# Optimization experiments

Hardware: AMD Instinct MI355X
Metric: run time of the kernel (lower is better)

The kernel has to match this reference:

```python
import jax, jax.numpy as jnp
import numpy as np

# dims: R ranks, B batch, HQ q-heads, HKV kv-heads-per-rank, G = HQ//HKV group size,
# D head dim, S kv splits (hardcoded 32 in module), L max kv len per rank, P pages per rank
R, B, HQ, HKV, D, S, L, P = 4, 16, 32, 2, 128, 32, 2048, 32768
G = HQ // HKV  # kv_group_num = num_q_heads // num_kv_heads_per_rank
NEG = -jnp.inf


def setup_inputs() -> dict:
    key = jax.random.key(0)
    k1, k2, k3, k4, k5 = jax.random.split(key, 5)
    q = jax.random.normal(k1, (B, HQ, D), jnp.float32)
    k_cache = jax.random.normal(k2, (R, P, HKV, D), jnp.float32)
    v_cache = jax.random.normal(k3, (R, P, HKV, D), jnp.float32)
    block_table = jax.random.randint(k4, (R, B, L), 0, P, jnp.int32)
    # per-rank kv lengths; min 64 to keep all math well-defined
    kv_lens_per_rank = jax.random.randint(k5, (R, B), 64, L + 1, jnp.int32)
    return dict(q=q, k_cache=k_cache, v_cache=v_cache,
                block_table=block_table, kv_lens_per_rank=kv_lens_per_rank)


def _attend(q, k_cache, v_cache, block_table, kv_lens):
    scale = D ** -0.5
    # page_size == 1: block_table entries are token slots in the per-rank cache.
    ridx = jnp.arange(R)[:, None, None]
    k = k_cache[ridx, block_table]  # [R,B,L,HKV,D]
    v = v_cache[ridx, block_table]  # [R,B,L,HKV,D]

    # GQA: q head h uses local kv head h // G on each rank
    qg = q.reshape(B, HKV, G, D)
    scores = jnp.einsum('bkgd,rblkd->rbkgl', qg, k) * scale  # [R,B,HKV,G,L]

    n = jnp.arange(L)
    valid = n[None, None, :] < kv_lens[..., None]            # [R,B,L]
    scores = jnp.where(valid[:, :, None, None, :], scores, NEG)

    # stage 1: split-KV. split s covers [s*per, (s+1)*per) with per = ceil(len/S)
    per = -(-kv_lens // S)                                   # [R,B]
    sid = n[None, None, :] // per[..., None]                 # [R,B,L]

    lse_s = []
    for s in range(S):  # fixed small loop over NUM_KV_SPLITS
        m = jnp.where((sid == s)[:, :, None, None, :], scores, NEG)
        lse_s.append(jax.scipy.special.logsumexp(m, axis=-1))  # [R,B,HKV,G]
    lse_s = jnp.stack(lse_s)  # [S,R,B,HKV,G]; empty splits -> -inf (kernel skips them)

    # stage 2: local combine over splits. NOTE (faithful to kernel): local_out stores
    # the UNNORMALIZED accumulator sum_s exp(lse_s - m_r) * o_s together with
    # lse_r = m_r + log(sum_s exp(lse_s - m_r)), where m_r = max_s lse_s.
    m_r = jnp.max(lse_s, axis=0)                              # [R,B,HKV,G]
    lse_r = m_r + jnp.log(jnp.sum(jnp.exp(lse_s - m_r), axis=0))
    # sum_s exp(lse_s - m_r) * (softmax_s @ v_s) == sum_n exp(score_n - m_r) * v_n
    p = jnp.exp(scores - m_r[..., None])                      # masked entries -> 0
    acc_r = jnp.einsum('rbkgl,rblkd->rbkgd', p, v)            # [R,B,HKV,G,D]

    acc = acc_r.reshape(R, B, HQ, D)
    lse = lse_r.reshape(R, B, HQ)

    # stage 3: global lse-weighted combine across ranks (online softmax == this)
    M = jnp.max(lse, axis=0)                                  # [B,HQ]
    w = jnp.exp(lse - M)                                      # [R,B,HQ]
    out = jnp.sum(w[..., None] * acc, axis=0) / jnp.sum(w, axis=0)[..., None]
    return out  # [B,HQ,D]


def reference(q, k_cache, v_cache, block_table, kv_lens_per_rank):
    return _attend(q, k_cache, v_cache, block_table, kv_lens_per_rank)
```

## Files before the change

### kernel.cpp

```cpp
#include <hip/hip_runtime.h>
#include <math.h>

#define R_ 4
#define B_ 16
#define HQ_ 32
#define HKV_ 2
#define G_ 16
#define D_ 128
#define S_ 32
#define L_ 2048
#define P_ 32768
#define TS_ 64
#define KSTR 136
#define PSTR 18
#define NEGINF (-INFINITY)

typedef _Float16 h4 __attribute__((ext_vector_type(4)));
typedef _Float16 h8 __attribute__((ext_vector_type(8)));
typedef float    fx4 __attribute__((ext_vector_type(4)));


__global__ __launch_bounds__(256, 8) void fd_stage1(
    const float* __restrict__ q, const float* __restrict__ kc,
    const float* __restrict__ vc, const int* __restrict__ bt,
    const int* __restrict__ lens,
    float* __restrict__ lse_split, float* __restrict__ chunk_m,
    _Float16* __restrict__ chunk_acc)
{
  const int t   = threadIdx.x;
  const int blk = blockIdx.x;
  const int s   = blk & 31;
  const int hkv = (blk >> 5) & 1;
  const int b   = (blk >> 6) & 15;
  const int r   = blk >> 10;

  const int len = lens[r*B_ + b];
  const int per = (len + 31) >> 5;
  const int n0  = s*per;
  const int tn  = min(per, len - n0);

  float* lse_out = lse_split + ((r*B_ + b)*HKV_ + hkv)*(S_*G_);
  const int cmbase = (((r*B_ + b)*HKV_ + hkv)*S_ + s)*G_;
  _Float16* ca = chunk_acc + (size_t)(((r*B_ + b)*HKV_ + hkv)*S_ + s)*(G_*D_);

  if (tn <= 0) {
    if (t < G_) { lse_out[s*G_ + t] = NEGINF; chunk_m[cmbase + t] = NEGINF; }
    h8 z = {};
    *(h8*)&ca[t*8] = z;
    return;
  }

  __shared__ _Float16 q_s[G_][KSTR];
  __shared__ __align__(16) float p_s[TS_][PSTR];
  __shared__ int pg_s[TS_];
  __shared__ float2 red_s[64];

  const int* btb   = bt + (r*B_ + b)*L_;
  const int kvbase = r*(P_*HKV_*D_) + hkv*D_;

  if (t < TS_) pg_s[t] = btb[n0 + t];

  {
    const float* qb = q + (b*HQ_ + hkv*G_)*D_;
    int fi = t;
    #pragma unroll
    for (int i = 0; i < 2; ++i, fi += 256) {
      const int g = fi >> 5, dd = (fi & 31)*4;
      const float4 v = *(const float4*)&qb[g*D_ + dd];
      h4 hv; hv.x=(_Float16)v.x; hv.y=(_Float16)v.y; hv.z=(_Float16)v.z; hv.w=(_Float16)v.w;
      *(h4*)&q_s[g][dd] = hv;
    }
  }
  __syncthreads();

  const int w  = t >> 6;
  const int l  = t & 63;
  const int hh = l & 15;
  const int tq = l >> 4;
  const bool active = (16*w) < tn;

  fx4 dacc = {0.f, 0.f, 0.f, 0.f};
  if (active) {
    const int row = 16*w + hh;
    const int pg  = pg_s[row];
    const float* kr = kc + kvbase + pg*(HKV_*D_) + 8*tq;
    #pragma unroll
    for (int c = 0; c < 4; ++c) {
      const float4 f0 = *(const float4*)&kr[c*32];
      const float4 f1 = *(const float4*)&kr[c*32 + 4];
      h8 af;
      af[0]=(_Float16)f0.x; af[1]=(_Float16)f0.y; af[2]=(_Float16)f0.z; af[3]=(_Float16)f0.w;
      af[4]=(_Float16)f1.x; af[5]=(_Float16)f1.y; af[6]=(_Float16)f1.z; af[7]=(_Float16)f1.w;
      const h8 bf = *(const h8*)&q_s[hh][c*32 + 8*tq];
      dacc = __builtin_amdgcn_mfma_f32_16x16x32_f16(af, bf, dacc, 0, 0, 0);
    }
  }

  const float sc = 0.08838834764831845f;
  const int nb = 16*w + 4*tq;
  const float sv0 = (nb + 0 < tn) ? dacc[0]*sc : NEGINF;
  const float sv1 = (nb + 1 < tn) ? dacc[1]*sc : NEGINF;
  const float sv2 = (nb + 2 < tn) ? dacc[2]*sc : NEGINF;
  const float sv3 = (nb + 3 < tn) ? dacc[3]*sc : NEGINF;

  float pmw = fmaxf(fmaxf(sv0, sv1), fmaxf(sv2, sv3));
  pmw = fmaxf(pmw, __shfl_xor(pmw, 16));
  pmw = fmaxf(pmw, __shfl_xor(pmw, 32));
  const float pms = (pmw == NEGINF) ? 0.f : pmw;
  const float e0 = __expf(sv0 - pms);
  const float e1 = __expf(sv1 - pms);
  const float e2 = __expf(sv2 - pms);
  const float e3 = __expf(sv3 - pms);
  float psw = e0 + e1 + e2 + e3;
  psw += __shfl_xor(psw, 16);
  psw += __shfl_xor(psw, 32);

  if (l < 16) red_s[w*16 + l] = make_float2(pmw, psw);
  __syncthreads();

  const float2 rr0 = red_s[hh], rr1 = red_s[16 + hh];
  const float2 rr2 = red_s[32 + hh], rr3 = red_s[48 + hh];
  const float pm = fmaxf(fmaxf(rr0.x, rr1.x), fmaxf(rr2.x, rr3.x));
  const float ps = rr0.y*__expf(rr0.x - pm) + rr1.y*__expf(rr1.x - pm)
                 + rr2.y*__expf(rr2.x - pm) + rr3.y*__expf(rr3.x - pm);

  if (w == 0 && l < 16) {
    lse_out[s*G_ + l]   = pm + __logf(ps);
    chunk_m[cmbase + l] = pm;
  }

  if (active) {
    const float cw = __expf(pmw - pm);
    p_s[nb + 0][hh] = e0*cw;
    p_s[nb + 1][hh] = e1*cw;
    p_s[nb + 2][hh] = e2*cw;
    p_s[nb + 3][hh] = e3*cw;
  }
  __syncthreads();

  const int d4 = (t & 31)*4;
  const int g2 = (t >> 5)*2;
  float4 a0 = make_float4(0.f,0.f,0.f,0.f);
  float4 a1 = make_float4(0.f,0.f,0.f,0.f);
  #pragma unroll 4
  for (int n = 0; n < tn; ++n) {
    const int pg = pg_s[n];
    const float4 v4 = *(const float4*)&vc[kvbase + pg*(HKV_*D_) + d4];
    const float2 pp = *(const float2*)&p_s[n][g2];
    a0.x += pp.x*v4.x; a0.y += pp.x*v4.y; a0.z += pp.x*v4.z; a0.w += pp.x*v4.w;
    a1.x += pp.y*v4.x; a1.y += pp.y*v4.y; a1.z += pp.y*v4.z; a1.w += pp.y*v4.w;
  }

  h4 o0; o0.x=(_Float16)a0.x; o0.y=(_Float16)a0.y; o0.z=(_Float16)a0.z; o0.w=(_Float16)a0.w;
  h4 o1; o1.x=(_Float16)a1.x; o1.y=(_Float16)a1.y; o1.z=(_Float16)a1.z; o1.w=(_Float16)a1.w;
  *(h4*)&ca[g2*D_ + d4]       = o0;
  *(h4*)&ca[(g2 + 1)*D_ + d4] = o1;
}

__global__ __launch_bounds__(128) void fd_stage2(
    const float* __restrict__ lse_split, const float* __restrict__ chunk_m,
    const _Float16* __restrict__ chunk_acc, float* __restrict__ out)
{
  const int bh  = blockIdx.x;
  const int b   = bh >> 5, h = bh & 31;
  const int hkv = h >> 4, g = h & 15;
  const int d   = threadIdx.x;

  float m_r[R_], lse_r[R_];
  #pragma unroll
  for (int r = 0; r < R_; ++r) {
    const float* ls = lse_split + ((r*B_ + b)*HKV_ + hkv)*(S_*G_) + g;
    float m = NEGINF;
    #pragma unroll 8
    for (int s2 = 0; s2 < S_; ++s2) m = fmaxf(m, ls[s2*G_]);
    float sum = 0.f;
    #pragma unroll 8
    for (int s2 = 0; s2 < S_; ++s2) sum += __expf(ls[s2*G_] - m);
    m_r[r]   = m;
    lse_r[r] = m + __logf(sum);
  }
  const float M = fmaxf(fmaxf(lse_r[0], lse_r[1]), fmaxf(lse_r[2], lse_r[3]));
  float denom = 0.f, o = 0.f;
  #pragma unroll
  for (int r = 0; r < R_; ++r) {
    const float w = __expf(lse_r[r] - M);
    denom += w;
    const float* cm = chunk_m + (((r*B_ + b)*HKV_ + hkv)*S_)*G_ + g;
    const _Float16* ca = chunk_acc
        + (size_t)(((r*B_ + b)*HKV_ + hkv)*S_)*(G_*D_) + g*D_ + d;
    float a = 0.f;
    #pragma unroll 8
    for (int c = 0; c < S_; ++c)
      a += __expf(cm[c*G_] - m_r[r]) * (float)ca[(size_t)c*(G_*D_)];
    o += w * a;
  }
  out[(size_t)bh*D_ + d] = o / denom;
}

extern "C" void kernel_launch(void* const* d_in, const int* in_sizes, int n_in,
                              void* d_out, int out_size, void* d_ws, size_t ws_size,
                              hipStream_t stream) {
  const float* q   = (const float*)d_in[0];
  const float* kc  = (const float*)d_in[1];
  const float* vc  = (const float*)d_in[2];
  const int*   bt  = (const int*)d_in[3];
  const int*   len = (const int*)d_in[4];
  float* out = (float*)d_out;
  float* ws  = (float*)d_ws;

  const size_t lse_f = (size_t)R_*B_*HKV_*S_*G_;
  float*    lse_split = ws;
  float*    chunk_m   = ws + lse_f;
  _Float16* chunk_acc = (_Float16*)(ws + 2*lse_f);

  fd_stage1<<<dim3(R_*B_*HKV_*S_), dim3(256), 0, stream>>>(
      q, kc, vc, bt, len, lse_split, chunk_m, chunk_acc);
  fd_stage2<<<dim3(B_*HQ_), dim3(128), 0, stream>>>(
      lse_split, chunk_m, chunk_acc, out);
}
```

Measured before the change: 300.5 us.

## Process both KV heads per stage-1 block to share page gathers

Stage 1 now handles both local KV heads in one block instead of one block per head, halving the grid. Each gathered page row is read for both heads at once, so K and V loads become contiguous 2×128 float spans and the block-table and page-index loads are shared. The cost is twice the MFMA and softmax work and more shared memory and registers per block, which may reduce occupancy and parallelism. A row bounds guard is added to the K loads.

```diff
diff --git a/kernel.cpp b/kernel.cpp
--- a/kernel.cpp
+++ b/kernel.cpp
@@ -30,45 +30,54 @@
   const int t   = threadIdx.x;
   const int blk = blockIdx.x;
   const int s   = blk & 31;
-  const int hkv = (blk >> 5) & 1;
-  const int b   = (blk >> 6) & 15;
-  const int r   = blk >> 10;
+  const int b   = (blk >> 5) & 15;
+  const int r   = blk >> 9;
 
   const int len = lens[r*B_ + b];
   const int per = (len + 31) >> 5;
   const int n0  = s*per;
   const int tn  = min(per, len - n0);
 
-  float* lse_out = lse_split + ((r*B_ + b)*HKV_ + hkv)*(S_*G_);
-  const int cmbase = (((r*B_ + b)*HKV_ + hkv)*S_ + s)*G_;
-  _Float16* ca = chunk_acc + (size_t)(((r*B_ + b)*HKV_ + hkv)*S_ + s)*(G_*D_);
+  const int rb = r*B_ + b;
+  float* lse0 = lse_split + (rb*HKV_ + 0)*(S_*G_) + s*G_;
+  float* lse1 = lse_split + (rb*HKV_ + 1)*(S_*G_) + s*G_;
+  float* cm0  = chunk_m   + ((rb*HKV_ + 0)*S_ + s)*G_;
+  float* cm1  = chunk_m   + ((rb*HKV_ + 1)*S_ + s)*G_;
+  _Float16* ca0 = chunk_acc + (size_t)((rb*HKV_ + 0)*S_ + s)*(G_*D_);
+  _Float16* ca1 = chunk_acc + (size_t)((rb*HKV_ + 1)*S_ + s)*(G_*D_);
 
   if (tn <= 0) {
-    if (t < G_) { lse_out[s*G_ + t] = NEGINF; chunk_m[cmbase + t] = NEGINF; }
+    if (t < 32) {
+      const int hk = t >> 4, g = t & 15;
+      (hk ? lse1 : lse0)[g] = NEGINF;
+      (hk ? cm1  : cm0 )[g] = NEGINF;
+    }
     h8 z = {};
-    *(h8*)&ca[t*8] = z;
+    *(h8*)&ca0[t*8] = z;
+    *(h8*)&ca1[t*8] = z;
     return;
   }
 
-  __shared__ _Float16 q_s[G_][KSTR];
-  __shared__ __align__(16) float p_s[TS_][PSTR];
-  __shared__ int pg_s[TS_];
-  __shared__ float2 red_s[64];
-
-  const int* btb   = bt + (r*B_ + b)*L_;
-  const int kvbase = r*(P_*HKV_*D_) + hkv*D_;
+  __shared__ _Float16 q_s[2][G_][KSTR];
+  __shared__ float    p_s[2][TS_][PSTR];
+  __shared__ int      pg_s[TS_];
+  __shared__ float2   red_s[2][64];
+
+  const int* btb = bt + rb*L_;
+  const float* kcb = kc + (size_t)r*(P_*HKV_*D_);
+  const float* vcb = vc + (size_t)r*(P_*HKV_*D_);
 
   if (t < TS_) pg_s[t] = btb[n0 + t];
 
   {
-    const float* qb = q + (b*HQ_ + hkv*G_)*D_;
+    const float* qb = q + b*HQ_*D_;
     int fi = t;
     #pragma unroll
-    for (int i = 0; i < 2; ++i, fi += 256) {
-      const int g = fi >> 5, dd = (fi & 31)*4;
-      const float4 v = *(const float4*)&qb[g*D_ + dd];
+    for (int i = 0; i < 4; ++i, fi += 256) {
+      const int h32 = fi >> 5, dd = (fi & 31)*4;
+      const float4 v = *(const float4*)&qb[h32*D_ + dd];
       h4 hv; hv.x=(_Float16)v.x; hv.y=(_Float16)v.y; hv.z=(_Float16)v.z; hv.w=(_Float16)v.w;
-      *(h4*)&q_s[g][dd] = hv;
+      *(h4*)&q_s[h32 >> 4][h32 & 15][dd] = hv;
     }
   }
   __syncthreads();
@@ -79,82 +88,129 @@
   const int tq = l >> 4;
   const bool active = (16*w) < tn;
 
-  fx4 dacc = {0.f, 0.f, 0.f, 0.f};
+  fx4 d0 = {0.f,0.f,0.f,0.f}, d1 = {0.f,0.f,0.f,0.f};
   if (active) {
     const int row = 16*w + hh;
-    const int pg  = pg_s[row];
-    const float* kr = kc + kvbase + pg*(HKV_*D_) + 8*tq;
+    const bool rowok = row < tn;
+    const int pg = pg_s[row];
+    const float* kr = kcb + pg*(HKV_*D_) + 8*tq;
     #pragma unroll
     for (int c = 0; c < 4; ++c) {
-      const float4 f0 = *(const float4*)&kr[c*32];
-      const float4 f1 = *(const float4*)&kr[c*32 + 4];
-      h8 af;
-      af[0]=(_Float16)f0.x; af[1]=(_Float16)f0.y; af[2]=(_Float16)f0.z; af[3]=(_Float16)f0.w;
-      af[4]=(_Float16)f1.x; af[5]=(_Float16)f1.y; af[6]=(_Float16)f1.z; af[7]=(_Float16)f1.w;
-      const h8 bf = *(const h8*)&q_s[hh][c*32 + 8*tq];
-      dacc = __builtin_amdgcn_mfma_f32_16x16x32_f16(af, bf, dacc, 0, 0, 0);
+      h8 a0 = {}, a1 = {};
+      if (rowok) {
+        const float4 f0 = *(const float4*)&kr[c*32];
+        const float4 f1 = *(const float4*)&kr[c*32 + 4];
+        const float4 f2 = *(const float4*)&kr[D_ + c*32];
+        const float4 f3 = *(const float4*)&kr[D_ + c*32 + 4];
+        a0[0]=(_Float16)f0.x; a0[1]=(_Float16)f0.y; a0[2]=(_Float16)f0.z; a0[3]=(_Float16)f0.w;
+        a0[4]=(_Float16)f1.x; a0[5]=(_Float16)f1.y; a0[6]=(_Float16)f1.z; a0[7]=(_Float16)f1.w;
+        a1[0]=(_Float16)f2.x; a1[1]=(_Float16)f2.y; a1[2]=(_Float16)f2.z; a1[3]=(_Float16)f2.w;
+        a1[4]=(_Float16)f3.x; a1[5]=(_Float16)f3.y; a1[6]=(_Float16)f3.z; a1[7]=(_Float16)f3.w;
+      }
+      const h8 b0 = *(const h8*)&q_s[0][hh][c*32 + 8*tq];
+      const h8 b1 = *(const h8*)&q_s[1][hh][c*32 + 8*tq];
+      d0 = __builtin_amdgcn_mfma_f32_16x16x32_f16(a0, b0, d0, 0, 0, 0);
+      d1 = __builtin_amdgcn_mfma_f32_16x16x32_f16(a1, b1, d1, 0, 0, 0);
     }
   }
 
   const float sc = 0.08838834764831845f;
   const int nb = 16*w + 4*tq;
-  const float sv0 = (nb + 0 < tn) ? dacc[0]*sc : NEGINF;
-  const float sv1 = (nb + 1 < tn) ? dacc[1]*sc : NEGINF;
-  const float sv2 = (nb + 2 < tn) ? dacc[2]*sc : NEGINF;
-  const float sv3 = (nb + 3 < tn) ? dacc[3]*sc : NEGINF;
-
-  float pmw = fmaxf(fmaxf(sv0, sv1), fmaxf(sv2, sv3));
-  pmw = fmaxf(pmw, __shfl_xor(pmw, 16));
-  pmw = fmaxf(pmw, __shfl_xor(pmw, 32));
-  const float pms = (pmw == NEGINF) ? 0.f : pmw;
-  const float e0 = __expf(sv0 - pms);
-  const float e1 = __expf(sv1 - pms);
-  const float e2 = __expf(sv2 - pms);
-  const float e3 = __expf(sv3 - pms);
-  float psw = e0 + e1 + e2 + e3;
-  psw += __shfl_xor(psw, 16);
-  psw += __shfl_xor(psw, 32);
-
-  if (l < 16) red_s[w*16 + l] = make_float2(pmw, psw);
+  float pm0w, ps0w, pm1w, ps1w;
+  float e00,e01,e02,e03, e10,e11,e12,e13;
+  {
+    const float s00 = (nb+0 < tn) ? d0[0]*sc : NEGINF;
+    const float s01 = (nb+1 < tn) ? d0[1]*sc : NEGINF;
+    const float s02 = (nb+2 < tn) ? d0[2]*sc : NEGINF;
+    const float s03 = (nb+3 < tn) ? d0[3]*sc : NEGINF;
+    float pm = fmaxf(fmaxf(s00,s01), fmaxf(s02,s03));
+    pm = fmaxf(pm, __shfl_xor(pm, 16));
+    pm = fmaxf(pm, __shfl_xor(pm, 32));
+    const float pms = (pm == NEGINF) ? 0.f : pm;
+    e00 = __expf(s00 - pms); e01 = __expf(s01 - pms);
+    e02 = __expf(s02 - pms); e03 = __expf(s03 - pms);
+    float ps = e00 + e01 + e02 + e03;
+    ps += __shfl_xor(ps, 16); ps += __shfl_xor(ps, 32);
+    pm0w = pm; ps0w = ps;
+  }
+  {
+    const float s10 = (nb+0 < tn) ? d1[0]*sc : NEGINF;
+    const float s11 = (nb+1 < tn) ? d1[1]*sc : NEGINF;
+    const float s12 = (nb+2 < tn) ? d1[2]*sc : NEGINF;
+    const float s13 = (nb+3 < tn) ? d1[3]*sc : NEGINF;
+    float pm = fmaxf(fmaxf(s10,s11), fmaxf(s12,s13));
+    pm = fmaxf(pm, __shfl_xor(pm, 16));
+    pm = fmaxf(pm, __shfl_xor(pm, 32));
+    const float pms = (pm == NEGINF) ? 0.f : pm;
+    e10 = __expf(s10 - pms); e11 = __expf(s11 - pms);
+    e12 = __expf(s12 - pms); e13 = __expf(s13 - pms);
+    float ps = e10 + e11 + e12 + e13;
+    ps += __shfl_xor(ps, 16); ps += __shfl_xor(ps, 32);
+    pm1w = pm; ps1w = ps;
+  }
+
+  if (l < 16) {
+    red_s[0][w*16 + l] = make_float2(pm0w, ps0w);
+    red_s[1][w*16 + l] = make_float2(pm1w, ps1w);
+  }
   __syncthreads();
 
-  const float2 rr0 = red_s[hh], rr1 = red_s[16 + hh];
-  const float2 rr2 = red_s[32 + hh], rr3 = red_s[48 + hh];
-  const float pm = fmaxf(fmaxf(rr0.x, rr1.x), fmaxf(rr2.x, rr3.x));
-  const float ps = rr0.y*__expf(rr0.x - pm) + rr1.y*__expf(rr1.x - pm)
-                 + rr2.y*__expf(rr2.x - pm) + rr3.y*__expf(rr3.x - pm);
-
-  if (w == 0 && l < 16) {
-    lse_out[s*G_ + l]   = pm + __logf(ps);
-    chunk_m[cmbase + l] = pm;
+  float pm0, pm1;
+  {
+    const float2 a = red_s[0][hh], c2 = red_s[0][16+hh];
+    const float2 e2 = red_s[0][32+hh], g2r = red_s[0][48+hh];
+    pm0 = fmaxf(fmaxf(a.x,c2.x), fmaxf(e2.x,g2r.x));
+    const float ps = a.y*__expf(a.x-pm0) + c2.y*__expf(c2.x-pm0)
+                   + e2.y*__expf(e2.x-pm0) + g2r.y*__expf(g2r.x-pm0);
+    if (w == 0 && l < 16) { lse0[l] = pm0 + __logf(ps); cm0[l] = pm0; }
+  }
+  {
+    const float2 a = red_s[1][hh], c2 = red_s[1][16+hh];
+    const float2 e2 = red_s[1][32+hh], g2r = red_s[1][48+hh];
+    pm1 = fmaxf(fmaxf(a.x,c2.x), fmaxf(e2.x,g2r.x));
+    const float ps = a.y*__expf(a.x-pm1) + c2.y*__expf(c2.x-pm1)
+                   + e2.y*__expf(e2.x-pm1) + g2r.y*__expf(g2r.x-pm1);
+    if (w == 1 && l < 16) { lse1[l] = pm1 + __logf(ps); cm1[l] = pm1; }
   }
 
   if (active) {
-    const float cw = __expf(pmw - pm);
-    p_s[nb + 0][hh] = e0*cw;
-    p_s[nb + 1][hh] = e1*cw;
-    p_s[nb + 2][hh] = e2*cw;
-    p_s[nb + 3][hh] = e3*cw;
+    const float c0 = __expf(pm0w - pm0);
+    const float c1 = __expf(pm1w - pm1);
+    p_s[0][nb+0][hh] = e00*c0; p_s[0][nb+1][hh] = e01*c0;
+    p_s[0][nb+2][hh] = e02*c0; p_s[0][nb+3][hh] = e03*c0;
+    p_s[1][nb+0][hh] = e10*c1; p_s[1][nb+1][hh] = e11*c1;
+    p_s[1][nb+2][hh] = e12*c1; p_s[1][nb+3][hh] = e13*c1;
   }
   __syncthreads();
 
+  const int hk = (t >> 5) & 1;
   const int d4 = (t & 31)*4;
-  const int g2 = (t >> 5)*2;
-  float4 a0 = make_float4(0.f,0.f,0.f,0.f);
-  float4 a1 = make_float4(0.f,0.f,0.f,0.f);
-  #pragma unroll 4
+  const float* vb = vcb + hk*D_ + d4;
+  const float* pp = &p_s[hk][0][4*w];
+  float4 a0 = make_float4(0,0,0,0), a1 = make_float4(0,0,0,0);
+  float4 a2 = make_float4(0,0,0,0), a3 = make_float4(0,0,0,0);
+  #pragma unroll 2
   for (int n = 0; n < tn; ++n) {
     const int pg = pg_s[n];
-    const float4 v4 = *(const float4*)&vc[kvbase + pg*(HKV_*D_) + d4];
-    const float2 pp = *(const float2*)&p_s[n][g2];
-    a0.x += pp.x*v4.x; a0.y += pp.x*v4.y; a0.z += pp.x*v4.z; a0.w += pp.x*v4.w;
-    a1.x += pp.y*v4.x; a1.y += pp.y*v4.y; a1.z += pp.y*v4.z; a1.w += pp.y*v4.w;
-  }
-
-  h4 o0; o0.x=(_Float16)a0.x; o0.y=(_Float16)a0.y; o0.z=(_Float16)a0.z; o0.w=(_Float16)a0.w;
-  h4 o1; o1.x=(_Float16)a1.x; o1.y=(_Float16)a1.y; o1.z=(_Float16)a1.z; o1.w=(_Float16)a1.w;
-  *(h4*)&ca[g2*D_ + d4]       = o0;
-  *(h4*)&ca[(g2 + 1)*D_ + d4] = o1;
+    const float4 v4 = *(const float4*)&vb[pg*(HKV_*D_)];
+    const float2 p01 = *(const float2*)&pp[n*PSTR];
+    const float2 p23 = *(const float2*)&pp[n*PSTR + 2];
+    a0.x += p01.x*v4.x; a0.y += p01.x*v4.y; a0.z += p01.x*v4.z; a0.w += p01.x*v4.w;
+    a1.x += p01.y*v4.x; a1.y += p01.y*v4.y; a1.z += p01.y*v4.z; a1.w += p01.y*v4.w;
+    a2.x += p23.x*v4.x; a2.y += p23.x*v4.y; a2.z += p23.x*v4.z; a2.w += p23.x*v4.w;
+    a3.x += p23.y*v4.x; a3.y += p23.y*v4.y; a3.z += p23.y*v4.z; a3.w += p23.y*v4.w;
+  }
+
+  _Float16* ca = hk ? ca1 : ca0;
+  h4 o;
+  o.x=(_Float16)a0.x; o.y=(_Float16)a0.y; o.z=(_Float16)a0.z; o.w=(_Float16)a0.w;
+  *(h4*)&ca[(4*w+0)*D_ + d4] = o;
+  o.x=(_Float16)a1.x; o.y=(_Float16)a1.y; o.z=(_Float16)a1.z; o.w=(_Float16)a1.w;
+  *(h4*)&ca[(4*w+1)*D_ + d4] = o;
+  o.x=(_Float16)a2.x; o.y=(_Float16)a2.y; o.z=(_Float16)a2.z; o.w=(_Float16)a2.w;
+  *(h4*)&ca[(4*w+2)*D_ + d4] = o;
+  o.x=(_Float16)a3.x; o.y=(_Float16)a3.y; o.z=(_Float16)a3.z; o.w=(_Float16)a3.w;
+  *(h4*)&ca[(4*w+3)*D_ + d4] = o;
 }
 
 __global__ __launch_bounds__(128) void fd_stage2(
@@ -213,7 +269,7 @@
   float*    chunk_m   = ws + lse_f;
   _Float16* chunk_acc = (_Float16*)(ws + 2*lse_f);
 
-  fd_stage1<<<dim3(R_*B_*HKV_*S_), dim3(256), 0, stream>>>(
+  fd_stage1<<<dim3(R_*B_*S_), dim3(256), 0, stream>>>(
       q, kc, vc, bt, len, lse_split, chunk_m, chunk_acc);
   fd_stage2<<<dim3(B_*HQ_), dim3(128), 0, stream>>>(
       lse_split, chunk_m, chunk_acc, out);
```

After: 300.6 us. About the same (+0.0%).

## Split each KV split into two 32-token chunks with 128-thread blocks

Applied to the files above, without the earlier changes.

Stage 1 now launches twice as many blocks: each KV split is divided into two 32-token chunks handled by 128-thread blocks. Each block writes its raw max and exp-sum, and stage 2 combines the sub-chunks and recomputes the per-split LSE. This spreads the gather-bound work over more, smaller blocks and adds more index math and a larger workspace in stage 2. The new block-index order puts hkv and the rank/batch index in the low bits, and empty chunks now skip zeroing their accumulator, with stage 2 checking for -inf instead.

```diff
diff --git a/kernel.cpp b/kernel.cpp
--- a/kernel.cpp
+++ b/kernel.cpp
@@ -8,11 +8,11 @@
 #define G_ 16
 #define D_ 128
 #define S_ 32
+#define CT_ 32
 #define L_ 2048
 #define P_ 32768
-#define TS_ 64
 #define KSTR 136
-#define PSTR 18
+#define PSTR 20
 #define NEGINF (-INFINITY)
 
 typedef _Float16 h4 __attribute__((ext_vector_type(4)));
@@ -20,51 +20,54 @@
 typedef float    fx4 __attribute__((ext_vector_type(4)));
 
 
-__global__ __launch_bounds__(256, 8) void fd_stage1(
+__global__ __launch_bounds__(128, 6) void fd_stage1(
     const float* __restrict__ q, const float* __restrict__ kc,
     const float* __restrict__ vc, const int* __restrict__ bt,
     const int* __restrict__ lens,
-    float* __restrict__ lse_split, float* __restrict__ chunk_m,
+    float* __restrict__ pm_ws, float* __restrict__ se_ws,
     _Float16* __restrict__ chunk_acc)
 {
   const int t   = threadIdx.x;
   const int blk = blockIdx.x;
-  const int s   = blk & 31;
-  const int hkv = (blk >> 5) & 1;
-  const int b   = (blk >> 6) & 15;
-  const int r   = blk >> 10;
-
-  const int len = lens[r*B_ + b];
+  const int c   = blk >> 12;
+  const int s   = (blk >> 7) & 31;
+  const int rb  = (blk >> 1) & 63;
+  const int hkv = blk & 1;
+  const int r   = rb >> 4, b = rb & 15;
+
+  const int len = lens[rb];
   const int per = (len + 31) >> 5;
-  const int n0  = s*per;
-  const int tn  = min(per, len - n0);
-
-  float* lse_out = lse_split + ((r*B_ + b)*HKV_ + hkv)*(S_*G_);
-  const int cmbase = (((r*B_ + b)*HKV_ + hkv)*S_ + s)*G_;
-  _Float16* ca = chunk_acc + (size_t)(((r*B_ + b)*HKV_ + hkv)*S_ + s)*(G_*D_);
+  const int sn0 = s*per;
+  const int stn = min(per, len - sn0);
+  const int n0  = sn0 + c*CT_;
+  const int tn  = min(stn - c*CT_, CT_);
+
+  const int widx = ((rb*HKV_ + hkv)*S_ + s)*2 + c;
+  float* pm_out = pm_ws + widx*G_;
+  float* se_out = se_ws + widx*G_;
+  _Float16* ca  = chunk_acc + (size_t)widx*(G_*D_);
 
   if (tn <= 0) {
-    if (t < G_) { lse_out[s*G_ + t] = NEGINF; chunk_m[cmbase + t] = NEGINF; }
-    h8 z = {};
-    *(h8*)&ca[t*8] = z;
+    if (t < G_) { pm_out[t] = NEGINF; se_out[t] = 0.f; }
     return;
   }
 
   __shared__ _Float16 q_s[G_][KSTR];
-  __shared__ __align__(16) float p_s[TS_][PSTR];
-  __shared__ int pg_s[TS_];
-  __shared__ float2 red_s[64];
-
-  const int* btb   = bt + (r*B_ + b)*L_;
-  const int kvbase = r*(P_*HKV_*D_) + hkv*D_;
-
-  if (t < TS_) pg_s[t] = btb[n0 + t];
+  __shared__ __align__(16) float p_s[CT_][PSTR];
+  __shared__ int      pg_s[CT_];
+  __shared__ float2   red_s[2][G_];
+
+  const int* btb = bt + rb*L_;
+  const float* kvk = kc + (size_t)r*(P_*HKV_*D_) + hkv*D_;
+  const float* kvv = vc + (size_t)r*(P_*HKV_*D_) + hkv*D_;
+
+  if (t < CT_) pg_s[t] = btb[n0 + t];
 
   {
     const float* qb = q + (b*HQ_ + hkv*G_)*D_;
     int fi = t;
     #pragma unroll
-    for (int i = 0; i < 2; ++i, fi += 256) {
+    for (int i = 0; i < 4; ++i, fi += 128) {
       const int g = fi >> 5, dd = (fi & 31)*4;
       const float4 v = *(const float4*)&qb[g*D_ + dd];
       h4 hv; hv.x=(_Float16)v.x; hv.y=(_Float16)v.y; hv.z=(_Float16)v.z; hv.w=(_Float16)v.w;
@@ -79,29 +82,32 @@
   const int tq = l >> 4;
   const bool active = (16*w) < tn;
 
-  fx4 dacc = {0.f, 0.f, 0.f, 0.f};
+  fx4 d0 = {0.f,0.f,0.f,0.f};
   if (active) {
     const int row = 16*w + hh;
-    const int pg  = pg_s[row];
-    const float* kr = kc + kvbase + pg*(HKV_*D_) + 8*tq;
+    const bool rowok = row < tn;
+    const int pg = pg_s[row];
+    const float* kr = kvk + pg*(HKV_*D_) + 8*tq;
     #pragma unroll
-    for (int c = 0; c < 4; ++c) {
-      const float4 f0 = *(const float4*)&kr[c*32];
-      const float4 f1 = *(const float4*)&kr[c*32 + 4];
-      h8 af;
-      af[0]=(_Float16)f0.x; af[1]=(_Float16)f0.y; af[2]=(_Float16)f0.z; af[3]=(_Float16)f0.w;
-      af[4]=(_Float16)f1.x; af[5]=(_Float16)f1.y; af[6]=(_Float16)f1.z; af[7]=(_Float16)f1.w;
-      const h8 bf = *(const h8*)&q_s[hh][c*32 + 8*tq];
-      dacc = __builtin_amdgcn_mfma_f32_16x16x32_f16(af, bf, dacc, 0, 0, 0);
+    for (int cc = 0; cc < 4; ++cc) {
+      h8 af = {};
+      if (rowok) {
+        const float4 f0 = *(const float4*)&kr[cc*32];
+        const float4 f1 = *(const float4*)&kr[cc*32 + 4];
+        af[0]=(_Float16)f0.x; af[1]=(_Float16)f0.y; af[2]=(_Float16)f0.z; af[3]=(_Float16)f0.w;
+        af[4]=(_Float16)f1.x; af[5]=(_Float16)f1.y; af[6]=(_Float16)f1.z; af[7]=(_Float16)f1.w;
+      }
+      const h8 bf = *(const h8*)&q_s[hh][cc*32 + 8*tq];
+      d0 = __builtin_amdgcn_mfma_f32_16x16x32_f16(af, bf, d0, 0, 0, 0);
     }
   }
 
   const float sc = 0.08838834764831845f;
   const int nb = 16*w + 4*tq;
-  const float sv0 = (nb + 0 < tn) ? dacc[0]*sc : NEGINF;
-  const float sv1 = (nb + 1 < tn) ? dacc[1]*sc : NEGINF;
-  const float sv2 = (nb + 2 < tn) ? dacc[2]*sc : NEGINF;
-  const float sv3 = (nb + 3 < tn) ? dacc[3]*sc : NEGINF;
+  const float sv0 = (nb+0 < tn) ? d0[0]*sc : NEGINF;
+  const float sv1 = (nb+1 < tn) ? d0[1]*sc : NEGINF;
+  const float sv2 = (nb+2 < tn) ? d0[2]*sc : NEGINF;
+  const float sv3 = (nb+3 < tn) ? d0[3]*sc : NEGINF;
 
   float pmw = fmaxf(fmaxf(sv0, sv1), fmaxf(sv2, sv3));
   pmw = fmaxf(pmw, __shfl_xor(pmw, 16));
@@ -115,50 +121,56 @@
   psw += __shfl_xor(psw, 16);
   psw += __shfl_xor(psw, 32);
 
-  if (l < 16) red_s[w*16 + l] = make_float2(pmw, psw);
+  if (l < 16) red_s[w][l] = make_float2(pmw, psw);
   __syncthreads();
 
-  const float2 rr0 = red_s[hh], rr1 = red_s[16 + hh];
-  const float2 rr2 = red_s[32 + hh], rr3 = red_s[48 + hh];
-  const float pm = fmaxf(fmaxf(rr0.x, rr1.x), fmaxf(rr2.x, rr3.x));
-  const float ps = rr0.y*__expf(rr0.x - pm) + rr1.y*__expf(rr1.x - pm)
-                 + rr2.y*__expf(rr2.x - pm) + rr3.y*__expf(rr3.x - pm);
+  const float2 r0 = red_s[0][hh], r1 = red_s[1][hh];
+  const float pm = fmaxf(r0.x, r1.x);
+  const float ps = r0.y*__expf(r0.x - pm) + r1.y*__expf(r1.x - pm);
 
   if (w == 0 && l < 16) {
-    lse_out[s*G_ + l]   = pm + __logf(ps);
-    chunk_m[cmbase + l] = pm;
+    pm_out[l] = pm;
+    se_out[l] = ps;
   }
 
   if (active) {
     const float cw = __expf(pmw - pm);
-    p_s[nb + 0][hh] = e0*cw;
-    p_s[nb + 1][hh] = e1*cw;
-    p_s[nb + 2][hh] = e2*cw;
-    p_s[nb + 3][hh] = e3*cw;
+    p_s[nb+0][hh] = e0*cw;
+    p_s[nb+1][hh] = e1*cw;
+    p_s[nb+2][hh] = e2*cw;
+    p_s[nb+3][hh] = e3*cw;
   }
   __syncthreads();
 
   const int d4 = (t & 31)*4;
-  const int g2 = (t >> 5)*2;
-  float4 a0 = make_float4(0.f,0.f,0.f,0.f);
-  float4 a1 = make_float4(0.f,0.f,0.f,0.f);
+  const int g4 = (t >> 5)*4;
+  const float* vb = kvv + d4;
+  float4 a0 = make_float4(0,0,0,0), a1 = make_float4(0,0,0,0);
+  float4 a2 = make_float4(0,0,0,0), a3 = make_float4(0,0,0,0);
   #pragma unroll 4
   for (int n = 0; n < tn; ++n) {
     const int pg = pg_s[n];
-    const float4 v4 = *(const float4*)&vc[kvbase + pg*(HKV_*D_) + d4];
-    const float2 pp = *(const float2*)&p_s[n][g2];
+    const float4 v4 = *(const float4*)&vb[pg*(HKV_*D_)];
+    const float4 pp = *(const float4*)&p_s[n][g4];
     a0.x += pp.x*v4.x; a0.y += pp.x*v4.y; a0.z += pp.x*v4.z; a0.w += pp.x*v4.w;
     a1.x += pp.y*v4.x; a1.y += pp.y*v4.y; a1.z += pp.y*v4.z; a1.w += pp.y*v4.w;
-  }
-
-  h4 o0; o0.x=(_Float16)a0.x; o0.y=(_Float16)a0.y; o0.z=(_Float16)a0.z; o0.w=(_Float16)a0.w;
-  h4 o1; o1.x=(_Float16)a1.x; o1.y=(_Float16)a1.y; o1.z=(_Float16)a1.z; o1.w=(_Float16)a1.w;
-  *(h4*)&ca[g2*D_ + d4]       = o0;
-  *(h4*)&ca[(g2 + 1)*D_ + d4] = o1;
+    a2.x += pp.z*v4.x; a2.y += pp.z*v4.y; a2.z += pp.z*v4.z; a2.w += pp.z*v4.w;
+    a3.x += pp.w*v4.x; a3.y += pp.w*v4.y; a3.z += pp.w*v4.z; a3.w += pp.w*v4.w;
+  }
+
+  h4 o;
+  o.x=(_Float16)a0.x; o.y=(_Float16)a0.y; o.z=(_Float16)a0.z; o.w=(_Float16)a0.w;
+  *(h4*)&ca[(g4+0)*D_ + d4] = o;
+  o.x=(_Float16)a1.x; o.y=(_Float16)a1.y; o.z=(_Float16)a1.z; o.w=(_Float16)a1.w;
+  *(h4*)&ca[(g4+1)*D_ + d4] = o;
+  o.x=(_Float16)a2.x; o.y=(_Float16)a2.y; o.z=(_Float16)a2.z; o.w=(_Float16)a2.w;
+  *(h4*)&ca[(g4+2)*D_ + d4] = o;
+  o.x=(_Float16)a3.x; o.y=(_Float16)a3.y; o.z=(_Float16)a3.z; o.w=(_Float16)a3.w;
+  *(h4*)&ca[(g4+3)*D_ + d4] = o;
 }
 
 __global__ __launch_bounds__(128) void fd_stage2(
-    const float* __restrict__ lse_split, const float* __restrict__ chunk_m,
+    const float* __restrict__ pm_ws, const float* __restrict__ se_ws,
     const _Float16* __restrict__ chunk_acc, float* __restrict__ out)
 {
   const int bh  = blockIdx.x;
@@ -169,13 +181,26 @@
   float m_r[R_], lse_r[R_];
   #pragma unroll
   for (int r = 0; r < R_; ++r) {
-    const float* ls = lse_split + ((r*B_ + b)*HKV_ + hkv)*(S_*G_) + g;
+    const int base = ((r*B_ + b)*HKV_ + hkv)*(S_*2);
     float m = NEGINF;
     #pragma unroll 8
-    for (int s2 = 0; s2 < S_; ++s2) m = fmaxf(m, ls[s2*G_]);
+    for (int s2 = 0; s2 < S_; ++s2) {
+      const float pm0 = pm_ws[(base + 2*s2    )*G_ + g];
+      const float pm1 = pm_ws[(base + 2*s2 + 1)*G_ + g];
+      const float pmx = fmaxf(pm0, pm1);
+      if (pmx > NEGINF) {
+        const float se0 = se_ws[(base + 2*s2    )*G_ + g];
+        const float se1 = se_ws[(base + 2*s2 + 1)*G_ + g];
+        const float tt = se0*__expf(pm0 - pmx) + se1*__expf(pm1 - pmx);
+        m = fmaxf(m, pmx + __logf(tt));
+      }
+    }
     float sum = 0.f;
     #pragma unroll 8
-    for (int s2 = 0; s2 < S_; ++s2) sum += __expf(ls[s2*G_] - m);
+    for (int sc2 = 0; sc2 < S_*2; ++sc2) {
+      const float pm = pm_ws[(base + sc2)*G_ + g];
+      if (pm > NEGINF) sum += se_ws[(base + sc2)*G_ + g]*__expf(pm - m);
+    }
     m_r[r]   = m;
     lse_r[r] = m + __logf(sum);
   }
@@ -185,13 +210,16 @@
   for (int r = 0; r < R_; ++r) {
     const float w = __expf(lse_r[r] - M);
     denom += w;
-    const float* cm = chunk_m + (((r*B_ + b)*HKV_ + hkv)*S_)*G_ + g;
-    const _Float16* ca = chunk_acc
-        + (size_t)(((r*B_ + b)*HKV_ + hkv)*S_)*(G_*D_) + g*D_ + d;
+    const int base = ((r*B_ + b)*HKV_ + hkv)*(S_*2);
     float a = 0.f;
-    #pragma unroll 8
-    for (int c = 0; c < S_; ++c)
-      a += __expf(cm[c*G_] - m_r[r]) * (float)ca[(size_t)c*(G_*D_)];
+    #pragma unroll 4
+    for (int sc2 = 0; sc2 < S_*2; ++sc2) {
+      const float pm = pm_ws[(base + sc2)*G_ + g];
+      if (pm > NEGINF) {
+        const float wc = __expf(pm - m_r[r]);
+        a += wc * (float)chunk_acc[(size_t)(base + sc2)*(G_*D_) + g*D_ + d];
+      }
+    }
     o += w * a;
   }
   out[(size_t)bh*D_ + d] = o / denom;
@@ -208,13 +236,13 @@
   float* out = (float*)d_out;
   float* ws  = (float*)d_ws;
 
-  const size_t lse_f = (size_t)R_*B_*HKV_*S_*G_;
-  float*    lse_split = ws;
-  float*    chunk_m   = ws + lse_f;
-  _Float16* chunk_acc = (_Float16*)(ws + 2*lse_f);
-
-  fd_stage1<<<dim3(R_*B_*HKV_*S_), dim3(256), 0, stream>>>(
-      q, kc, vc, bt, len, lse_split, chunk_m, chunk_acc);
+  const size_t nt = (size_t)R_*B_*HKV_*S_*2;
+  float*    pm_ws     = ws;
+  float*    se_ws     = ws + nt*G_;
+  _Float16* chunk_acc = (_Float16*)(ws + 2*nt*G_);
+
+  fd_stage1<<<dim3(2*S_*64*HKV_ ), dim3(128), 0, stream>>>(
+      q, kc, vc, bt, len, pm_ws, se_ws, chunk_acc);
   fd_stage2<<<dim3(B_*HQ_), dim3(128), 0, stream>>>(
-      lse_split, chunk_m, chunk_acc, out);
+      pm_ws, se_ws, chunk_acc, out);
 }
```

Measured after the change: 476.9 us. 1.59x slower.
